# Kernel tuning notes

Hardware: AMD Instinct MI355X
Metric: run time of the kernel (lower is better)

## Reference

```python
import jax, jax.numpy as jnp
import numpy as np

B, D, H, F, L, M, MEM, ACT, STO, HID = 2048, 1024, 8, 4096, 2, 256, 16, 32, 1024, 1024
HD = D // H
SCALE = HD ** -0.5
EPS = 1e-4


def rmsnorm(x, w):
    return x * jax.lax.rsqrt(jnp.mean(x * x, axis=-1, keepdims=True) + EPS) * w


def setup_inputs() -> dict:
    key = jax.random.key(0)
    ks = iter(jax.random.split(key, 32))

    def nrm(shape, scale=0.02):
        return jax.random.normal(next(ks), shape, dtype=jnp.float32) * scale

    return {
        'stoch': jax.random.normal(next(ks), (B, STO), dtype=jnp.float32),
        'deter': jax.random.normal(next(ks), (B, D), dtype=jnp.float32),
        'action': jax.random.normal(next(ks), (B, ACT), dtype=jnp.float32),
        'memory': jax.random.normal(next(ks), (B, MEM, D), dtype=jnp.float32),
        'inp_w1': nrm((STO + ACT, HID)), 'inp_b1': jnp.zeros((HID,), jnp.float32),
        'inp_nw': jnp.ones((HID,), jnp.float32),
        'inp_w2': nrm((HID, D)), 'inp_b2': jnp.zeros((D,), jnp.float32),
        'Wq': nrm((L, D, D)), 'bq': jnp.zeros((L, D), jnp.float32),
        'Wk': nrm((L, D, D)), 'bk': jnp.zeros((L, D), jnp.float32),
        'Wv': nrm((L, D, D)), 'bv': jnp.zeros((L, D), jnp.float32),
        'Wo': nrm((L, D, D)), 'bo': jnp.zeros((L, D), jnp.float32),
        'rel_emb': nrm((L, 2 * M + 1, H)),
        'n1w': jnp.ones((L, D), jnp.float32), 'n2w': jnp.ones((L, D), jnp.float32),
        'ffw1': nrm((L, D, F)), 'ffb1': jnp.zeros((L, F), jnp.float32),
        'ffw2': nrm((L, F, D)), 'ffb2': jnp.zeros((L, D), jnp.float32),
        'fnw': jnp.ones((D,), jnp.float32),
    }


def reference(stoch, deter, action, memory, inp_w1, inp_b1, inp_nw, inp_w2, inp_b2,
              Wq, bq, Wk, bk, Wv, bv, Wo, bo, rel_emb, n1w, n2w,
              ffw1, ffb1, ffw2, ffb2, fnw):
    # action normalization: denominator is detached in torch
    a = action / jax.lax.stop_gradient(jnp.maximum(jnp.abs(action), 1.0))
    tok = jnp.concatenate([stoch.reshape(stoch.shape[0], -1), a], axis=-1)
    tok = jax.nn.silu(rmsnorm(tok @ inp_w1 + inp_b1, inp_nw)) @ inp_w2 + inp_b2  # [B,D]
    seq = jnp.concatenate([memory, tok[:, None, :]], axis=1)  # [B,S,D], S = MEM+1
    S = seq.shape[1]
    rel = jnp.clip(jnp.arange(S)[:, None] - jnp.arange(S)[None, :], -M, M) + M  # [S,S]
    for l in range(L):
        xn = rmsnorm(seq, n1w[l])
        q = (xn @ Wq[l] + bq[l]).reshape(-1, S, H, HD)
        k = (xn @ Wk[l] + bk[l]).reshape(-1, S, H, HD)
        v = (xn @ Wv[l] + bv[l]).reshape(-1, S, H, HD)
        bias = rel_emb[l][rel].transpose(2, 0, 1)  # [H,S,S]
        scores = jnp.einsum('bqhd,bkhd->bhqk', q, k) * SCALE + bias[None]
        probs = jax.nn.softmax(scores, axis=-1)
        att = jnp.einsum('bhqk,bkhd->bqhd', probs, v).reshape(-1, S, D)
        seq = seq + (att @ Wo[l] + bo[l])
        xn2 = rmsnorm(seq, n2w[l])
        seq = seq + (jax.nn.gelu(xn2 @ ffw1[l] + ffb1[l], approximate=False) @ ffw2[l] + ffb2[l])
    new_deter = rmsnorm(seq[:, -1] + deter, fnw)
    new_mem = jax.lax.stop_gradient(seq[:, -MEM:])
    return (new_deter, new_mem)
```

## Files before the change

### kernel.cpp

```cpp
#include <hip/hip_runtime.h>
#include <hip/hip_bf16.h>
#include <math.h>

#define NB 2048
#define ND 1024
#define NH 8
#define NHD 128
#define NF 4096
#define NL 2
#define NMEM 16
#define NS 17
#define NROWS (NB*NS)
#define NTOK 1056
#define SCALE_ATT 0.08838834764831845f

typedef unsigned short u16;
typedef unsigned int u32;

typedef __bf16 bf16x8 __attribute__((ext_vector_type(8)));
typedef float f32x4 __attribute__((ext_vector_type(4)));

__device__ __forceinline__ float bf2f(u16 h) {
  union { u32 u; float f; } c; c.u = ((u32)h) << 16; return c.f;
}
__device__ __forceinline__ u16 f2bf(float f) {
  union { float ff; u32 u; } c; c.ff = f;
  return (u16)((c.u + 0x7FFFu + ((c.u >> 16) & 1u)) >> 16);
}
__device__ __forceinline__ bf16x8 as_b8(uint4 u) {
  union { uint4 u; bf16x8 b; } c; c.u = u; return c.b;
}

__device__ __forceinline__ void gload16(const void* g, void* l) {
  __builtin_amdgcn_global_load_lds(
      (const __attribute__((address_space(1))) void*)(uintptr_t)g,
      (__attribute__((address_space(3))) void*)(u32)(uintptr_t)l,
      16, 0, 0);
}

__global__ __launch_bounds__(256)
void pack_wT_k(const float* __restrict__ src, u16* __restrict__ dst, int K, int N)
{
  __shared__ float tile[32][33];
  int tx = threadIdx.x & 31, ty = threadIdx.x >> 5;
  int n0 = blockIdx.x * 32, k0 = blockIdx.y * 32;
#pragma unroll
  for (int r = ty; r < 32; r += 8)
    tile[r][tx] = src[(size_t)(k0 + r) * N + n0 + tx];
  __syncthreads();
#pragma unroll
  for (int r = ty; r < 32; r += 8)
    dst[(size_t)(n0 + r) * K + k0 + tx] = f2bf(tile[tx][r]);
}

__global__ __launch_bounds__(256)
void pack_bqkv_k(const float* __restrict__ bq, const float* __restrict__ bk,
                 const float* __restrict__ bv, float* __restrict__ dst)
{
  int j = blockIdx.x * 256 + threadIdx.x;
  if (j >= 3072) return;
  float v = (j < 1024) ? bq[j] : (j < 2048 ? bk[j - 1024] : bv[j - 2048]);
  dst[j] = v;
}

template<int EPI>
__global__ __launch_bounds__(256)
void gemm2_k(const u16* __restrict__ A, int lda,
             const u16* __restrict__ BT, int ldb,
             const float* __restrict__ bias,
             u16* __restrict__ Cb, float* __restrict__ Cf, int ldc,
             int K)
{
  __shared__ __align__(16) u16 Asm[2][128 * 32];
  __shared__ __align__(16) u16 Bsm[2][128 * 32];
  const int tid  = threadIdx.x;
  const int lane = tid & 63;
  const int wv   = tid >> 6;
  const int wm   = wv >> 1, wn = wv & 1;
  const int lr   = lane & 15;
  const int kb   = lane >> 4;

  const int gx = gridDim.x;
  const int nwg = gx * gridDim.y;
  int bid = blockIdx.y * gx + blockIdx.x;
  if ((nwg & 7) == 0) bid = (bid & 7) * (nwg >> 3) + (bid >> 3);
  const int bx = bid % gx, by = bid / gx;
  const long bmBase = (long)by * 128;
  const int  bnBase = bx * 128;

  const int srow = tid >> 2;
  const int skc  = ((tid & 3) ^ ((srow >> 1) & 3)) * 8;
  const u16* aG0 = A  + (size_t)(bmBase + srow) * lda + skc;
  const u16* aG1 = aG0 + (size_t)64 * lda;
  const u16* bG0 = BT + (size_t)(bnBase + srow) * ldb + skc;
  const u16* bG1 = bG0 + (size_t)64 * ldb;
  const int wbase = (tid & ~63) * 8;

  const int rslot = (kb ^ ((lr >> 1) & 3)) * 8;

  f32x4 acc[4][4];
#pragma unroll
  for (int m = 0; m < 4; ++m)
#pragma unroll
    for (int n = 0; n < 4; ++n)
      acc[m][n] = (f32x4){0.0f, 0.0f, 0.0f, 0.0f};

  const int nk = K >> 5;

  {
    u16* aL = &Asm[0][wbase];
    u16* bL = &Bsm[0][wbase];
    gload16(aG0, aL);
    gload16(aG1, aL + 2048);
    gload16(bG0, bL);
    gload16(bG1, bL + 2048);
  }
  asm volatile("s_waitcnt vmcnt(0)" ::: "memory");
  __builtin_amdgcn_s_barrier();

  for (int i = 0; i < nk; ++i) {
    const int cur = i & 1;
    if (i + 1 < nk) {
      const int kt = (i + 1) << 5;
      u16* aL = &Asm[cur ^ 1][wbase];
      u16* bL = &Bsm[cur ^ 1][wbase];
      gload16(aG0 + kt, aL);
      gload16(aG1 + kt, aL + 2048);
      gload16(bG0 + kt, bL);
      gload16(bG1 + kt, bL + 2048);
    }

    bf16x8 af[4], bfv[4];
#pragma unroll
    for (int m = 0; m < 4; ++m)
      af[m] = as_b8(*(const uint4*)&Asm[cur][(wm * 64 + m * 16 + lr) * 32 + rslot]);
#pragma unroll
    for (int n = 0; n < 4; ++n)
      bfv[n] = as_b8(*(const uint4*)&Bsm[cur][(wn * 64 + n * 16 + lr) * 32 + rslot]);
#pragma unroll
    for (int m = 0; m < 4; ++m)
#pragma unroll
      for (int n = 0; n < 4; ++n)
        acc[m][n] = __builtin_amdgcn_mfma_f32_16x16x32_bf16(af[m], bfv[n], acc[m][n], 0, 0, 0);

    asm volatile("s_waitcnt vmcnt(0)" ::: "memory");
    __builtin_amdgcn_s_barrier();
  }

#pragma unroll
  for (int m = 0; m < 4; ++m) {
#pragma unroll
    for (int n = 0; n < 4; ++n) {
      int gcol = bnBase + wn * 64 + n * 16 + lr;
      float bv = bias[gcol];
      long growb = bmBase + wm * 64 + m * 16 + (lane >> 4) * 4;
#pragma unroll
      for (int i = 0; i < 4; ++i) {
        float val = acc[m][n][i] + bv;
        long row = growb + i;
        if (EPI == 1) val = 0.5f * val * (1.0f + erff(val * 0.70710678118654752f));
        if (EPI == 0 || EPI == 1) {
          Cb[(size_t)row * ldc + gcol] = f2bf(val);
        } else if (EPI == 2) {
          float* p = Cf + (size_t)row * ldc + gcol;
          *p = *p + val;
        } else {
          Cf[(size_t)row * ldc + gcol] = val;
        }
      }
    }
  }
}

__global__ __launch_bounds__(256)
void prep_tokcat_k(const float* __restrict__ stoch, const float* __restrict__ action,
                   u16* __restrict__ tok)
{
  size_t idx = (size_t)blockIdx.x * 256 + threadIdx.x;
  if (idx >= (size_t)NB * NTOK) return;
  int b = (int)(idx / NTOK), j = (int)(idx % NTOK);
  float v;
  if (j < 1024) {
    v = stoch[(size_t)b * 1024 + j];
  } else {
    float a = action[(size_t)b * 32 + (j - 1024)];
    v = a / fmaxf(fabsf(a), 1.0f);
  }
  tok[idx] = f2bf(v);
}

__global__ __launch_bounds__(256)
void rmsnorm_f32_k(const float* __restrict__ X, const float* __restrict__ w,
                   u16* __restrict__ Y)
{
  int row = blockIdx.x;
  const float* x = X + (size_t)row * 1024;
  int t = threadIdx.x;
  float4 v = *(const float4*)&x[t * 4];
  float ss = v.x * v.x + v.y * v.y + v.z * v.z + v.w * v.w;
#pragma unroll
  for (int o = 1; o < 64; o <<= 1) ss += __shfl_xor(ss, o, 64);
  __shared__ float red[4];
  if ((t & 63) == 0) red[t >> 6] = ss;
  __syncthreads();
  float tot = red[0] + red[1] + red[2] + red[3];
  float r = rsqrtf(tot * (1.0f / 1024.0f) + 1e-4f);
  float4 wv = *(const float4*)&w[t * 4];
  union { u16 s[4]; uint2 u; } ob;
  ob.s[0] = f2bf(v.x * r * wv.x);
  ob.s[1] = f2bf(v.y * r * wv.y);
  ob.s[2] = f2bf(v.z * r * wv.z);
  ob.s[3] = f2bf(v.w * r * wv.w);
  *(uint2*)&Y[(size_t)row * 1024 + t * 4] = ob.u;
}

__global__ __launch_bounds__(256)
void rmsnorm_silu_k(u16* __restrict__ X, const float* __restrict__ w)
{
  int row = blockIdx.x;
  u16* x = X + (size_t)row * 1024;
  int t = threadIdx.x;
  union { u16 s[4]; uint2 u; } iv;
  iv.u = *(uint2*)&x[t * 4];
  float v0 = bf2f(iv.s[0]), v1 = bf2f(iv.s[1]), v2 = bf2f(iv.s[2]), v3 = bf2f(iv.s[3]);
  float ss = v0 * v0 + v1 * v1 + v2 * v2 + v3 * v3;
#pragma unroll
  for (int o = 1; o < 64; o <<= 1) ss += __shfl_xor(ss, o, 64);
  __shared__ float red[4];
  if ((t & 63) == 0) red[t >> 6] = ss;
  __syncthreads();
  float tot = red[0] + red[1] + red[2] + red[3];
  float r = rsqrtf(tot * (1.0f / 1024.0f) + 1e-4f);
  float4 wv = *(const float4*)&w[t * 4];
  float n0 = v0 * r * wv.x;
  float n1 = v1 * r * wv.y;
  float n2 = v2 * r * wv.z;
  float n3 = v3 * r * wv.w;
  union { u16 s[4]; uint2 u; } ob;
  ob.s[0] = f2bf(n0 / (1.0f + expf(-n0)));
  ob.s[1] = f2bf(n1 / (1.0f + expf(-n1)));
  ob.s[2] = f2bf(n2 / (1.0f + expf(-n2)));
  ob.s[3] = f2bf(n3 / (1.0f + expf(-n3)));
  *(uint2*)&x[t * 4] = ob.u;
}

__global__ __launch_bounds__(256)
void init_seq_k(const float* __restrict__ mem, float* __restrict__ seq)
{
  size_t idx = ((size_t)blockIdx.x * 256 + threadIdx.x) * 4;
  if (idx >= (size_t)NB * 16 * 1024) return;
  size_t b = idx / (16 * 1024), rem = idx % (16 * 1024);
  float4 v = *(const float4*)&mem[idx];
  *(float4*)&seq[b * (size_t)NS * 1024 + rem] = v;
}

__global__ __launch_bounds__(256)
void copy_mem_k(const float* __restrict__ seq, float* __restrict__ out)
{
  size_t idx = ((size_t)blockIdx.x * 256 + threadIdx.x) * 4;
  if (idx >= (size_t)NB * 16 * 1024) return;
  size_t b = idx / (16 * 1024), rem = idx % (16 * 1024);
  float4 v = *(const float4*)&seq[b * (size_t)NS * 1024 + 1024 + rem];
  *(float4*)&out[idx] = v;
}

__global__ __launch_bounds__(256)
void final_deter_k(const float* __restrict__ seq, const float* __restrict__ deter,
                   const float* __restrict__ fnw, float* __restrict__ out)
{
  int b = blockIdx.x;
  const float* xs = seq + ((size_t)b * NS + 16) * 1024;
  const float* dt = deter + (size_t)b * 1024;
  int t = threadIdx.x;
  float v[4];
#pragma unroll
  for (int j = 0; j < 4; ++j) v[j] = xs[t * 4 + j] + dt[t * 4 + j];
  float ss = v[0] * v[0] + v[1] * v[1] + v[2] * v[2] + v[3] * v[3];
#pragma unroll
  for (int o = 1; o < 64; o <<= 1) ss += __shfl_xor(ss, o, 64);
  __shared__ float red[4];
  if ((t & 63) == 0) red[t >> 6] = ss;
  __syncthreads();
  float tot = red[0] + red[1] + red[2] + red[3];
  float r = rsqrtf(tot * (1.0f / 1024.0f) + 1e-4f);
  float4 ov;
  ov.x = v[0] * r * fnw[t * 4 + 0];
  ov.y = v[1] * r * fnw[t * 4 + 1];
  ov.z = v[2] * r * fnw[t * 4 + 2];
  ov.w = v[3] * r * fnw[t * 4 + 3];
  *(float4*)&out[(size_t)b * 1024 + t * 4] = ov;
}

#define LSTR 132
__global__ __launch_bounds__(256)
void attn_k(const u16* __restrict__ QKV, const float* __restrict__ rel,
            u16* __restrict__ O)
{
  __shared__ float qs[NS * LSTR];
  __shared__ float ks[NS * LSTR];
  __shared__ float vs[NS * LSTR];
  __shared__ float sc[NS * 20];
  int bh = blockIdx.x;
  int b = bh >> 3, h = bh & 7;
  int t = threadIdx.x;
  const size_t rowb = (size_t)b * NS * 3072 + h * 128;
  for (int e4 = t; e4 < NS * 32; e4 += 256) {
    int i = e4 >> 5, d = (e4 & 31) * 4;
    size_t off = rowb + (size_t)i * 3072 + d;
    uint2 q2 = *(const uint2*)(QKV + off);
    uint2 k2 = *(const uint2*)(QKV + off + 1024);
    uint2 v2 = *(const uint2*)(QKV + off + 2048);
    const u16* qp = (const u16*)&q2;
    const u16* kp = (const u16*)&k2;
    const u16* vp = (const u16*)&v2;
#pragma unroll
    for (int j = 0; j < 4; ++j) {
      qs[i * LSTR + d + j] = bf2f(qp[j]);
      ks[i * LSTR + d + j] = bf2f(kp[j]);
      vs[i * LSTR + d + j] = bf2f(vp[j]);
    }
  }
  __syncthreads();
  for (int e = t; e < NS * NS; e += 256) {
    int i = e / NS, j = e % NS;
    const float4* q4 = (const float4*)&qs[i * LSTR];
    const float4* k4 = (const float4*)&ks[j * LSTR];
    float s = 0.0f;
#pragma unroll
    for (int dd = 0; dd < 32; ++dd) {
      float4 a = q4[dd], bb = k4[dd];
      s += a.x * bb.x + a.y * bb.y + a.z * bb.z + a.w * bb.w;
    }
    sc[i * 20 + j] = s * SCALE_ATT + rel[(i - j + 256) * 8 + h];
  }
  __syncthreads();
  if (t < NS) {
    float mx = -1e30f;
    for (int j = 0; j < NS; ++j) mx = fmaxf(mx, sc[t * 20 + j]);
    float sum = 0.0f;
    for (int j = 0; j < NS; ++j) { float e = expf(sc[t * 20 + j] - mx); sc[t * 20 + j] = e; sum += e; }
    float inv = 1.0f / sum;
    for (int j = 0; j < NS; ++j) sc[t * 20 + j] *= inv;
  }
  __syncthreads();
  const size_t obase = (size_t)b * NS * 1024 + h * 128;
  for (int e = t; e < NS * 128; e += 256) {
    int i = e >> 7, d = e & 127;
    float o = 0.0f;
#pragma unroll
    for (int j = 0; j < NS; ++j) o += sc[i * 20 + j] * vs[j * LSTR + d];
    O[obase + (size_t)i * 1024 + d] = f2bf(o);
  }
}

extern "C" void kernel_launch(void* const* d_in, const int* in_sizes, int n_in,
                              void* d_out, int out_size, void* d_ws, size_t ws_size,
                              hipStream_t stream)
{
  const float* stoch  = (const float*)d_in[0];
  const float* deter  = (const float*)d_in[1];
  const float* action = (const float*)d_in[2];
  const float* memory = (const float*)d_in[3];
  const float* inp_w1 = (const float*)d_in[4];
  const float* inp_b1 = (const float*)d_in[5];
  const float* inp_nw = (const float*)d_in[6];
  const float* inp_w2 = (const float*)d_in[7];
  const float* inp_b2 = (const float*)d_in[8];
  const float* Wq = (const float*)d_in[9];
  const float* bq = (const float*)d_in[10];
  const float* Wk = (const float*)d_in[11];
  const float* bk = (const float*)d_in[12];
  const float* Wv = (const float*)d_in[13];
  const float* bv = (const float*)d_in[14];
  const float* Wo = (const float*)d_in[15];
  const float* bo = (const float*)d_in[16];
  const float* rel_emb = (const float*)d_in[17];
  const float* n1w = (const float*)d_in[18];
  const float* n2w = (const float*)d_in[19];
  const float* ffw1 = (const float*)d_in[20];
  const float* ffb1 = (const float*)d_in[21];
  const float* ffw2 = (const float*)d_in[22];
  const float* ffb2 = (const float*)d_in[23];
  const float* fnw  = (const float*)d_in[24];
  float* out = (float*)d_out;

  char* ws = (char*)d_ws;
  float* SEQ = (float*)ws;
  u16* XN  = (u16*)(ws + 142606336ULL);
  u16* QKV = (u16*)(ws + 213909504ULL);
  u16* FFH = QKV;
  u16* TOK = (u16*)(ws + 427819008ULL);
  u16* H1  = (u16*)(ws + 432144384ULL);
  u16* PK  = (u16*)(ws + 436338688ULL);
  float* BQKV = (float*)(ws + 461504512ULL);
  if (ws_size < 461516800ULL) return;

  dim3 blk(256);

  u16* w1T = PK;
  u16* w2T = PK + 1024 * 1056;
  pack_wT_k<<<dim3(1024 / 32, 1056 / 32), blk, 0, stream>>>(inp_w1, w1T, NTOK, 1024);
  pack_wT_k<<<dim3(1024 / 32, 1024 / 32), blk, 0, stream>>>(inp_w2, w2T, 1024, 1024);
  prep_tokcat_k<<<(NB * NTOK + 255) / 256, blk, 0, stream>>>(stoch, action, TOK);
  gemm2_k<0><<<dim3(8, 16), blk, 0, stream>>>(TOK, NTOK, w1T, NTOK, inp_b1, H1, nullptr, 1024, NTOK);
  rmsnorm_silu_k<<<NB, blk, 0, stream>>>(H1, inp_nw);
  gemm2_k<3><<<dim3(8, 16), blk, 0, stream>>>(H1, 1024, w2T, 1024, inp_b2, nullptr, SEQ + 16 * 1024, NS * 1024, 1024);
  init_seq_k<<<(NB * 16 * 1024 / 4 + 255) / 256, blk, 0, stream>>>(memory, SEQ);

  u16* qkvT = PK;
  u16* oT  = PK + 3145728;
  u16* f1T = PK + 4194304;
  u16* f2T = PK + 8388608;

  for (int l = 0; l < NL; ++l) {
    const float* wq = Wq + (size_t)l * ND * ND;
    const float* wk = Wk + (size_t)l * ND * ND;
    const float* wv = Wv + (size_t)l * ND * ND;
    const float* wo = Wo + (size_t)l * ND * ND;
    const float* w1 = ffw1 + (size_t)l * ND * NF;
    const float* w2 = ffw2 + (size_t)l * NF * ND;
    const float* rl = rel_emb + (size_t)l * 513 * NH;

    pack_wT_k<<<dim3(32, 32), blk, 0, stream>>>(wq, qkvT, 1024, 1024);
    pack_wT_k<<<dim3(32, 32), blk, 0, stream>>>(wk, qkvT + 1048576, 1024, 1024);
    pack_wT_k<<<dim3(32, 32), blk, 0, stream>>>(wv, qkvT + 2097152, 1024, 1024);
    pack_wT_k<<<dim3(32, 32), blk, 0, stream>>>(wo, oT, 1024, 1024);
    pack_wT_k<<<dim3(128, 32), blk, 0, stream>>>(w1, f1T, 1024, 4096);
    pack_wT_k<<<dim3(32, 128), blk, 0, stream>>>(w2, f2T, 4096, 1024);
    pack_bqkv_k<<<12, blk, 0, stream>>>(bq + l * ND, bk + l * ND, bv + l * ND, BQKV);

    rmsnorm_f32_k<<<NROWS, blk, 0, stream>>>(SEQ, n1w + l * ND, XN);
    gemm2_k<0><<<dim3(24, 272), blk, 0, stream>>>(XN, 1024, qkvT, 1024, BQKV, QKV, nullptr, 3072, 1024);
    attn_k<<<NB * NH, blk, 0, stream>>>(QKV, rl, XN);
    gemm2_k<2><<<dim3(8, 272), blk, 0, stream>>>(XN, 1024, oT, 1024, bo + l * ND, nullptr, SEQ, 1024, 1024);
    rmsnorm_f32_k<<<NROWS, blk, 0, stream>>>(SEQ, n2w + l * ND, XN);
    for (int c = 0; c < 2; ++c) {
      size_t r0 = (size_t)c * 17408;
      gemm2_k<1><<<dim3(32, 136), blk, 0, stream>>>(XN + r0 * 1024, 1024, f1T, 1024, ffb1 + l * NF, FFH, nullptr, 4096, 1024);
      gemm2_k<2><<<dim3(8, 136), blk, 0, stream>>>(FFH, 4096, f2T, 4096, ffb2 + l * ND, nullptr, SEQ + r0 * 1024, 1024, 4096);
    }
  }

  final_deter_k<<<NB, blk, 0, stream>>>(SEQ, deter, fnw, out);
  copy_mem_k<<<(NB * 16 * 1024 / 4 + 255) / 256, blk, 0, stream>>>(SEQ, out + (size_t)NB * ND);
}
```

Before: 3.447 ms.

## Fuse per-layer weight packing into one launch and use wave-per-row rmsnorm

Replaces the seven per-layer weight-transpose and bias-pack launches with a single kernel that dispatches on block index. Rewrites both rmsnorm kernels so each wave handles one row with 16 elements per lane, removing the shared-memory reduction and barrier and using 16-byte loads and stores. Widens the attention kernel's QKV staging loads from 8 to 16 bytes. These target launch overhead and memory-access efficiency in the small kernels; the dominant GEMMs are unchanged.

```diff
diff --git a/kernel.cpp b/kernel.cpp
--- a/kernel.cpp
+++ b/kernel.cpp
@@ -38,29 +38,56 @@
       16, 0, 0);
 }
 
+__device__ __forceinline__ void pack_tile(const float* __restrict__ src,
+                                          u16* __restrict__ dst,
+                                          int K, int N, int n0, int k0,
+                                          float* tile )
+{
+  int tx = threadIdx.x & 31, ty = threadIdx.x >> 5;
+#pragma unroll
+  for (int r = ty; r < 32; r += 8)
+    tile[r * 33 + tx] = src[(size_t)(k0 + r) * N + n0 + tx];
+  __syncthreads();
+#pragma unroll
+  for (int r = ty; r < 32; r += 8)
+    dst[(size_t)(n0 + r) * K + k0 + tx] = f2bf(tile[tx * 33 + r]);
+}
+
 __global__ __launch_bounds__(256)
 void pack_wT_k(const float* __restrict__ src, u16* __restrict__ dst, int K, int N)
 {
-  __shared__ float tile[32][33];
-  int tx = threadIdx.x & 31, ty = threadIdx.x >> 5;
-  int n0 = blockIdx.x * 32, k0 = blockIdx.y * 32;
-#pragma unroll
-  for (int r = ty; r < 32; r += 8)
-    tile[r][tx] = src[(size_t)(k0 + r) * N + n0 + tx];
-  __syncthreads();
-#pragma unroll
-  for (int r = ty; r < 32; r += 8)
-    dst[(size_t)(n0 + r) * K + k0 + tx] = f2bf(tile[tx][r]);
-}
-
-__global__ __launch_bounds__(256)
-void pack_bqkv_k(const float* __restrict__ bq, const float* __restrict__ bk,
-                 const float* __restrict__ bv, float* __restrict__ dst)
-{
-  int j = blockIdx.x * 256 + threadIdx.x;
-  if (j >= 3072) return;
-  float v = (j < 1024) ? bq[j] : (j < 2048 ? bk[j - 1024] : bv[j - 2048]);
-  dst[j] = v;
+  __shared__ float tile[32 * 33];
+  pack_tile(src, dst, K, N, blockIdx.x * 32, blockIdx.y * 32, tile);
+}
+
+__global__ __launch_bounds__(256)
+void pack_layer_k(const float* __restrict__ wq, const float* __restrict__ wk,
+                  const float* __restrict__ wv, const float* __restrict__ wo,
+                  const float* __restrict__ w1, const float* __restrict__ w2,
+                  const float* __restrict__ bq, const float* __restrict__ bk,
+                  const float* __restrict__ bv,
+                  u16* __restrict__ qkvT, u16* __restrict__ oT,
+                  u16* __restrict__ f1T, u16* __restrict__ f2T,
+                  float* __restrict__ BQKV)
+{
+  __shared__ float tile[32 * 33];
+  int id = blockIdx.x;
+  if (id < 4096) {
+    int which = id >> 10, l = id & 1023;
+    const float* src = which == 0 ? wq : which == 1 ? wk : which == 2 ? wv : wo;
+    u16* dst = which == 3 ? oT : qkvT + (size_t)which * 1048576;
+    pack_tile(src, dst, 1024, 1024, (l & 31) * 32, (l >> 5) * 32, tile);
+  } else if (id < 8192) {
+    int l = id - 4096;
+    pack_tile(w1, f1T, 1024, 4096, (l & 127) * 32, (l >> 7) * 32, tile);
+  } else if (id < 12288) {
+    int l = id - 8192;
+    pack_tile(w2, f2T, 4096, 1024, (l & 31) * 32, (l >> 5) * 32, tile);
+  } else {
+    int j = (id - 12288) * 256 + threadIdx.x;
+    if (j < 3072)
+      BQKV[j] = (j < 1024) ? bq[j] : (j < 2048 ? bk[j - 1024] : bv[j - 2048]);
+  }
 }
 
 template<int EPI>
@@ -95,7 +122,6 @@
   const u16* bG0 = BT + (size_t)(bnBase + srow) * ldb + skc;
   const u16* bG1 = bG0 + (size_t)64 * ldb;
   const int wbase = (tid & ~63) * 8;
-
   const int rslot = (kb ^ ((lr >> 1) & 3)) * 8;
 
   f32x4 acc[4][4];
@@ -106,7 +132,6 @@
       acc[m][n] = (f32x4){0.0f, 0.0f, 0.0f, 0.0f};
 
   const int nk = K >> 5;
-
   {
     u16* aL = &Asm[0][wbase];
     u16* bL = &Bsm[0][wbase];
@@ -129,7 +154,6 @@
       gload16(bG0 + kt, bL);
       gload16(bG1 + kt, bL + 2048);
     }
-
     bf16x8 af[4], bfv[4];
 #pragma unroll
     for (int m = 0; m < 4; ++m)
@@ -142,7 +166,6 @@
 #pragma unroll
       for (int n = 0; n < 4; ++n)
         acc[m][n] = __builtin_amdgcn_mfma_f32_16x16x32_bf16(af[m], bfv[n], acc[m][n], 0, 0, 0);
-
     asm volatile("s_waitcnt vmcnt(0)" ::: "memory");
     __builtin_amdgcn_s_barrier();
   }
@@ -193,55 +216,59 @@
 void rmsnorm_f32_k(const float* __restrict__ X, const float* __restrict__ w,
                    u16* __restrict__ Y)
 {
-  int row = blockIdx.x;
-  const float* x = X + (size_t)row * 1024;
-  int t = threadIdx.x;
-  float4 v = *(const float4*)&x[t * 4];
-  float ss = v.x * v.x + v.y * v.y + v.z * v.z + v.w * v.w;
+  const int wv = threadIdx.x >> 6, lane = threadIdx.x & 63;
+  const size_t row = (size_t)blockIdx.x * 4 + wv;
+  const float* x = X + row * 1024 + lane * 16;
+  float4 v[4];
+#pragma unroll
+  for (int j = 0; j < 4; ++j) v[j] = ((const float4*)x)[j];
+  float ss = 0.0f;
+#pragma unroll
+  for (int j = 0; j < 4; ++j)
+    ss += v[j].x * v[j].x + v[j].y * v[j].y + v[j].z * v[j].z + v[j].w * v[j].w;
 #pragma unroll
   for (int o = 1; o < 64; o <<= 1) ss += __shfl_xor(ss, o, 64);
-  __shared__ float red[4];
-  if ((t & 63) == 0) red[t >> 6] = ss;
-  __syncthreads();
-  float tot = red[0] + red[1] + red[2] + red[3];
-  float r = rsqrtf(tot * (1.0f / 1024.0f) + 1e-4f);
-  float4 wv = *(const float4*)&w[t * 4];
-  union { u16 s[4]; uint2 u; } ob;
-  ob.s[0] = f2bf(v.x * r * wv.x);
-  ob.s[1] = f2bf(v.y * r * wv.y);
-  ob.s[2] = f2bf(v.z * r * wv.z);
-  ob.s[3] = f2bf(v.w * r * wv.w);
-  *(uint2*)&Y[(size_t)row * 1024 + t * 4] = ob.u;
+  const float r = rsqrtf(ss * (1.0f / 1024.0f) + 1e-4f);
+  const float* wp = w + lane * 16;
+  union { u16 s[16]; uint4 u[2]; } ob;
+#pragma unroll
+  for (int j = 0; j < 4; ++j) {
+    float4 wj = ((const float4*)wp)[j];
+    ob.s[j * 4 + 0] = f2bf(v[j].x * r * wj.x);
+    ob.s[j * 4 + 1] = f2bf(v[j].y * r * wj.y);
+    ob.s[j * 4 + 2] = f2bf(v[j].z * r * wj.z);
+    ob.s[j * 4 + 3] = f2bf(v[j].w * r * wj.w);
+  }
+  uint4* dst = (uint4*)(Y + row * 1024 + lane * 16);
+  dst[0] = ob.u[0];
+  dst[1] = ob.u[1];
 }
 
 __global__ __launch_bounds__(256)
 void rmsnorm_silu_k(u16* __restrict__ X, const float* __restrict__ w)
 {
-  int row = blockIdx.x;
-  u16* x = X + (size_t)row * 1024;
-  int t = threadIdx.x;
-  union { u16 s[4]; uint2 u; } iv;
-  iv.u = *(uint2*)&x[t * 4];
-  float v0 = bf2f(iv.s[0]), v1 = bf2f(iv.s[1]), v2 = bf2f(iv.s[2]), v3 = bf2f(iv.s[3]);
-  float ss = v0 * v0 + v1 * v1 + v2 * v2 + v3 * v3;
+  const int wv = threadIdx.x >> 6, lane = threadIdx.x & 63;
+  const size_t row = (size_t)blockIdx.x * 4 + wv;
+  u16* x = X + row * 1024 + lane * 16;
+  union { u16 s[16]; uint4 u[2]; } iv;
+  iv.u[0] = ((const uint4*)x)[0];
+  iv.u[1] = ((const uint4*)x)[1];
+  float f[16];
+  float ss = 0.0f;
+#pragma unroll
+  for (int j = 0; j < 16; ++j) { f[j] = bf2f(iv.s[j]); ss += f[j] * f[j]; }
 #pragma unroll
   for (int o = 1; o < 64; o <<= 1) ss += __shfl_xor(ss, o, 64);
-  __shared__ float red[4];
-  if ((t & 63) == 0) red[t >> 6] = ss;
-  __syncthreads();
-  float tot = red[0] + red[1] + red[2] + red[3];
-  float r = rsqrtf(tot * (1.0f / 1024.0f) + 1e-4f);
-  float4 wv = *(const float4*)&w[t * 4];
-  float n0 = v0 * r * wv.x;
-  float n1 = v1 * r * wv.y;
-  float n2 = v2 * r * wv.z;
-  float n3 = v3 * r * wv.w;
-  union { u16 s[4]; uint2 u; } ob;
-  ob.s[0] = f2bf(n0 / (1.0f + expf(-n0)));
-  ob.s[1] = f2bf(n1 / (1.0f + expf(-n1)));
-  ob.s[2] = f2bf(n2 / (1.0f + expf(-n2)));
-  ob.s[3] = f2bf(n3 / (1.0f + expf(-n3)));
-  *(uint2*)&x[t * 4] = ob.u;
+  const float r = rsqrtf(ss * (1.0f / 1024.0f) + 1e-4f);
+  const float* wp = w + lane * 16;
+  union { u16 s[16]; uint4 u[2]; } ob;
+#pragma unroll
+  for (int j = 0; j < 16; ++j) {
+    float n = f[j] * r * wp[j];
+    ob.s[j] = f2bf(n / (1.0f + expf(-n)));
+  }
+  ((uint4*)x)[0] = ob.u[0];
+  ((uint4*)x)[1] = ob.u[1];
 }
 
 __global__ __launch_bounds__(256)
@@ -304,17 +331,17 @@
   int b = bh >> 3, h = bh & 7;
   int t = threadIdx.x;
   const size_t rowb = (size_t)b * NS * 3072 + h * 128;
-  for (int e4 = t; e4 < NS * 32; e4 += 256) {
-    int i = e4 >> 5, d = (e4 & 31) * 4;
+  for (int e = t; e < NS * 16; e += 256) {
+    int i = e >> 4, d = (e & 15) * 8;
     size_t off = rowb + (size_t)i * 3072 + d;
-    uint2 q2 = *(const uint2*)(QKV + off);
-    uint2 k2 = *(const uint2*)(QKV + off + 1024);
-    uint2 v2 = *(const uint2*)(QKV + off + 2048);
-    const u16* qp = (const u16*)&q2;
-    const u16* kp = (const u16*)&k2;
-    const u16* vp = (const u16*)&v2;
-#pragma unroll
-    for (int j = 0; j < 4; ++j) {
+    uint4 q4 = *(const uint4*)(QKV + off);
+    uint4 k4 = *(const uint4*)(QKV + off + 1024);
+    uint4 v4 = *(const uint4*)(QKV + off + 2048);
+    const u16* qp = (const u16*)&q4;
+    const u16* kp = (const u16*)&k4;
+    const u16* vp = (const u16*)&v4;
+#pragma unroll
+    for (int j = 0; j < 8; ++j) {
       qs[i * LSTR + d + j] = bf2f(qp[j]);
       ks[i * LSTR + d + j] = bf2f(kp[j]);
       vs[i * LSTR + d + j] = bf2f(vp[j]);
@@ -403,7 +430,7 @@
   pack_wT_k<<<dim3(1024 / 32, 1024 / 32), blk, 0, stream>>>(inp_w2, w2T, 1024, 1024);
   prep_tokcat_k<<<(NB * NTOK + 255) / 256, blk, 0, stream>>>(stoch, action, TOK);
   gemm2_k<0><<<dim3(8, 16), blk, 0, stream>>>(TOK, NTOK, w1T, NTOK, inp_b1, H1, nullptr, 1024, NTOK);
-  rmsnorm_silu_k<<<NB, blk, 0, stream>>>(H1, inp_nw);
+  rmsnorm_silu_k<<<NB / 4, blk, 0, stream>>>(H1, inp_nw);
   gemm2_k<3><<<dim3(8, 16), blk, 0, stream>>>(H1, 1024, w2T, 1024, inp_b2, nullptr, SEQ + 16 * 1024, NS * 1024, 1024);
   init_seq_k<<<(NB * 16 * 1024 / 4 + 255) / 256, blk, 0, stream>>>(memory, SEQ);
 
@@ -421,19 +448,15 @@
     const float* w2 = ffw2 + (size_t)l * NF * ND;
     const float* rl = rel_emb + (size_t)l * 513 * NH;
 
-    pack_wT_k<<<dim3(32, 32), blk, 0, stream>>>(wq, qkvT, 1024, 1024);
-    pack_wT_k<<<dim3(32, 32), blk, 0, stream>>>(wk, qkvT + 1048576, 1024, 1024);
-    pack_wT_k<<<dim3(32, 32), blk, 0, stream>>>(wv, qkvT + 2097152, 1024, 1024);
-    pack_wT_k<<<dim3(32, 32), blk, 0, stream>>>(wo, oT, 1024, 1024);
-    pack_wT_k<<<dim3(128, 32), blk, 0, stream>>>(w1, f1T, 1024, 4096);
-    pack_wT_k<<<dim3(32, 128), blk, 0, stream>>>(w2, f2T, 4096, 1024);
-    pack_bqkv_k<<<12, blk, 0, stream>>>(bq + l * ND, bk + l * ND, bv + l * ND, BQKV);
-
-    rmsnorm_f32_k<<<NROWS, blk, 0, stream>>>(SEQ, n1w + l * ND, XN);
+    pack_layer_k<<<12300, blk, 0, stream>>>(wq, wk, wv, wo, w1, w2,
+                                            bq + l * ND, bk + l * ND, bv + l * ND,
+                                            qkvT, oT, f1T, f2T, BQKV);
+
+    rmsnorm_f32_k<<<NROWS / 4, blk, 0, stream>>>(SEQ, n1w + l * ND, XN);
     gemm2_k<0><<<dim3(24, 272), blk, 0, stream>>>(XN, 1024, qkvT, 1024, BQKV, QKV, nullptr, 3072, 1024);
     attn_k<<<NB * NH, blk, 0, stream>>>(QKV, rl, XN);
     gemm2_k<2><<<dim3(8, 272), blk, 0, stream>>>(XN, 1024, oT, 1024, bo + l * ND, nullptr, SEQ, 1024, 1024);
-    rmsnorm_f32_k<<<NROWS, blk, 0, stream>>>(SEQ, n2w + l * ND, XN);
+    rmsnorm_f32_k<<<NROWS / 4, blk, 0, stream>>>(SEQ, n2w + l * ND, XN);
     for (int c = 0; c < 2; ++c) {
       size_t r0 = (size_t)c * 17408;
       gemm2_k<1><<<dim3(32, 136), blk, 0, stream>>>(XN + r0 * 1024, 1024, f1T, 1024, ffb1 + l * NF, FFH, nullptr, 4096, 1024);
```

After: 3.401 ms. Within noise of the previous version (-1.3%).
